# Optimization experiments

Hardware: AMD Instinct MI355X
Metric: run time of the kernel (lower is better)

## Reference

```python
import jax, jax.numpy as jnp
import numpy as np

TOP_K = 2
NUM_EXPERTS = 8
CAPACITY_FACTOR = 1.0


def setup_inputs() -> dict:
    key = jax.random.key(0)
    k1, k2, k3, k4 = jax.random.split(key, 4)
    sl, bs, hs, ffn = 2048, 2, 1024, 4096
    x = jax.random.normal(k1, (sl, bs, hs), dtype=jnp.float32)
    router_w = jax.random.normal(k2, (hs, NUM_EXPERTS), dtype=jnp.float32) * 0.02
    w1 = jax.random.normal(k3, (NUM_EXPERTS, hs, ffn), dtype=jnp.float32) * 0.02
    w2 = jax.random.normal(k4, (NUM_EXPERTS, ffn, hs), dtype=jnp.float32) * 0.02
    bias = jnp.zeros((1, 1, hs), dtype=jnp.float32)
    return {"x": x, "router_w": router_w, "w1": w1, "w2": w2, "bias": bias}


def _moe_forward(x, router_w, w1, w2):
    sl, bs, hs = x.shape
    xf = x.reshape(-1, hs)                                   # [T, H]
    T = xf.shape[0]
    TK = T * TOP_K
    capacity = int(CAPACITY_FACTOR * TOP_K * T / NUM_EXPERTS)  # static

    # Router: softmax over experts, then top-k (LearnedRouter)
    scores = jax.nn.softmax(xf @ router_w, axis=-1)          # [T, E]
    expert_weights, top_experts = jax.lax.top_k(scores, TOP_K)  # [T, K]
    ew = expert_weights.reshape(-1)                          # [T*K]
    te = top_experts.reshape(-1).astype(jnp.int32)           # [T*K]

    # indices_and_bins: stable sort by expert id + histogram + inclusive cumsum
    indices = jnp.argsort(te, stable=True)                   # sorted pos -> flat slot
    tokens_per_expert = jnp.zeros((NUM_EXPERTS,), jnp.int32).at[te].add(1)
    bins = jnp.cumsum(tokens_per_expert)                     # inclusive cumsum
    starts = bins - tokens_per_expert                        # exclusive offsets

    # binned_gather -> [E, capacity, H]; tokens beyond capacity are dropped
    c_range = jnp.arange(capacity)
    pos = starts[:, None] + c_range[None, :]                 # [E, C] positions in sorted order
    valid = c_range[None, :] < tokens_per_expert[:, None]    # [E, C]
    slot = indices[jnp.clip(pos, 0, TK - 1)]                 # flat (token*K + k) slot
    tok = slot // TOP_K                                      # source token row
    gathered = jnp.where(valid[..., None], xf[tok], 0.0)     # [E, C, H]

    # grouped expert MLP: gelu(x @ w1) @ w2  (megablocks mlp.MLP)
    h = jax.nn.gelu(jnp.einsum('ech,ehf->ecf', gathered, w1))
    y = jnp.einsum('ecf,efh->ech', h, w2)                    # [E, C, H]

    # binned_scatter: weighted accumulate back to token rows
    p = jnp.arange(TK)
    e_of_p = jnp.searchsorted(bins, p, side='right')         # expert of sorted pos
    c_of_p = p - starts[e_of_p]                              # slot within expert bin
    ok = c_of_p < capacity                                   # dropped tokens contribute 0
    vals = jnp.where(ok[:, None], y[e_of_p, jnp.clip(c_of_p, 0, capacity - 1)], 0.0)
    flat = indices                                           # flat slot at sorted pos p
    w = ew[flat]
    out = jnp.zeros((T, hs), x.dtype).at[flat // TOP_K].add(w[:, None] * vals)
    return out.reshape(sl, bs, hs)


def reference(x, router_w, w1, w2, bias):
    out = _moe_forward(x, router_w, w1, w2)
    return (out, bias)
```

## Files before the change

### kernel.cpp

```cpp
#include <hip/hip_runtime.h>
#include <hip/hip_bf16.h>


#define T_TOK 4096
#define HS 1024
#define FFN 4096
#define NE 8
#define CAP 1024
#define TKS 8192

#define WS_TE   67108864
#define WS_EW   67141632
#define WS_PERM 67174400
#define WS_WT   67239936
#define WS_XB   134348800

typedef float f4 __attribute__((ext_vector_type(4)));
typedef __bf16 bf16x8 __attribute__((ext_vector_type(8)));
typedef float f32x4 __attribute__((ext_vector_type(4)));

__device__ __forceinline__ void gld_lds16(const void* g, void* l) {
    __builtin_amdgcn_global_load_lds(
        (const __attribute__((address_space(1))) unsigned int*)g,
        (__attribute__((address_space(3))) unsigned int*)l, 16, 0, 0);
}

__global__ void init_out_kernel(float* __restrict__ out, const float* __restrict__ bias) {
    int i = blockIdx.x * 256 + threadIdx.x;
    const int TH = T_TOK * HS;
    if (i < TH) out[i] = 0.0f;
    else if (i < TH + HS) out[i] = bias[i - TH];
}

__global__ __launch_bounds__(256) void router_kernel(const float* __restrict__ x,
                                                     const float* __restrict__ rw,
                                                     int* __restrict__ te,
                                                     float* __restrict__ ew,
                                                     __bf16* __restrict__ xb) {
    __shared__ float rwt[NE * HS];
    int tid = threadIdx.x;
    for (int i = tid; i < NE * HS; i += 256) {
        int h = i >> 3, e = i & 7;
        rwt[e * HS + h] = rw[i];
    }
    __syncthreads();
    int wave = tid >> 6, lane = tid & 63;
    int t = blockIdx.x * 4 + wave;
    const float* xr = x + (size_t)t * HS;
    float s[NE];
    float xv[16];
#pragma unroll
    for (int e = 0; e < NE; ++e) s[e] = 0.0f;
#pragma unroll
    for (int j = 0; j < 16; ++j) {
        int h = lane + j * 64;
        xv[j] = xr[h];
#pragma unroll
        for (int e = 0; e < NE; ++e) s[e] += xv[j] * rwt[e * HS + h];
    }
#pragma unroll
    for (int j = 0; j < 16; ++j)
        xb[(size_t)t * HS + lane + j * 64] = (__bf16)xv[j];
#pragma unroll
    for (int e = 0; e < NE; ++e) {
#pragma unroll
        for (int off = 1; off < 64; off <<= 1) s[e] += __shfl_xor(s[e], off, 64);
    }
    float m = s[0];
#pragma unroll
    for (int e = 1; e < NE; ++e) m = fmaxf(m, s[e]);
    float psum = 0.0f;
#pragma unroll
    for (int e = 0; e < NE; ++e) psum += __expf(s[e] - m);
    int e0 = 0; float v0 = s[0];
#pragma unroll
    for (int e = 1; e < NE; ++e) { if (s[e] > v0) { v0 = s[e]; e0 = e; } }
    int e1 = -1; float v1 = -1e30f;
#pragma unroll
    for (int e = 0; e < NE; ++e) { if (e != e0 && s[e] > v1) { v1 = s[e]; e1 = e; } }
    if (lane == 0) {
        float inv = 1.0f / psum;
        te[2 * t]     = e0;
        te[2 * t + 1] = e1;
        ew[2 * t]     = __expf(v0 - m) * inv;
        ew[2 * t + 1] = __expf(v1 - m) * inv;
    }
}

__global__ __launch_bounds__(256) void sort_kernel(const int* __restrict__ te,
                                                   int* __restrict__ perm) {
    __shared__ int hist[256 * NE];
    int tid = threadIdx.x;
#pragma unroll
    for (int e = 0; e < NE; ++e) hist[tid * NE + e] = 0;
    for (int i = tid; i < TKS; i += 256) perm[i] = -1;
    __syncthreads();
    for (int j = 0; j < 32; ++j) {
        int p = tid * 32 + j;
        hist[tid * NE + te[p]]++;
    }
    __syncthreads();
    if (tid < NE) {
        int run = 0;
        for (int i = 0; i < 256; ++i) {
            int v = hist[i * NE + tid];
            hist[i * NE + tid] = run;
            run += v;
        }
    }
    __syncthreads();
    for (int j = 0; j < 32; ++j) {
        int p = tid * 32 + j;
        int e = te[p];
        int c = hist[tid * NE + e]++;
        if (c < CAP) perm[e * CAP + c] = p;
    }
}

__global__ __launch_bounds__(256) void conv_wt_kernel(const float* __restrict__ w,
                                                      __bf16* __restrict__ wt,
                                                      int K, int N) {
    __shared__ __bf16 t[64][72];
    const int e = blockIdx.z;
    const int kb = blockIdx.y * 64, nb = blockIdx.x * 64;
    const int tid = threadIdx.x;
    const float* src = w + ((size_t)e * K + kb) * N + nb;
    {
        const int kk = tid >> 4, nc = (tid & 15) * 4;
#pragma unroll
        for (int i = 0; i < 4; ++i) {
            int k = kk + 16 * i;
            f4 v = *(const f4*)(src + (size_t)k * N + nc);
            t[nc + 0][k] = (__bf16)v[0];
            t[nc + 1][k] = (__bf16)v[1];
            t[nc + 2][k] = (__bf16)v[2];
            t[nc + 3][k] = (__bf16)v[3];
        }
    }
    __syncthreads();
    __bf16* dst = wt + ((size_t)e * N + nb) * K + kb;
    const int nn = tid >> 3, ch = (tid & 7) * 8;
#pragma unroll
    for (int i = 0; i < 2; ++i) {
        int n = nn + 32 * i;
        bf16x8 v = *(const bf16x8*)(&t[n][ch]);
        *(bf16x8*)(dst + (size_t)n * K + ch) = v;
    }
}


#define PBAR() do {                                                         \
    asm volatile("" ::: "memory");                                          \
    __builtin_amdgcn_s_barrier();                                           \
    asm volatile("" ::: "memory");                                          \
} while (0)

#define WAITV(N_) asm volatile("s_waitcnt vmcnt(" #N_ ")" ::: "memory")

#define STAGE_A(cb_, h_, koff_) do {                                        \
    gld_lds16(aptr[(h_)*2 + 0] + (koff_), &As[cb_][(h_)*128 + w*16 + 0][0]);\
    gld_lds16(aptr[(h_)*2 + 1] + (koff_), &As[cb_][(h_)*128 + w*16 + 8][0]);\
} while (0)

#define STAGE_B(cb_, h_, koff_) do {                                        \
    gld_lds16(bptr[(h_)*2 + 0] + (koff_), &Bs[cb_][(h_)*128 + w*16 + 0][0]);\
    gld_lds16(bptr[(h_)*2 + 1] + (koff_), &Bs[cb_][(h_)*128 + w*16 + 8][0]);\
} while (0)

#define RD_A4(MB_) do {                                                     \
    _Pragma("unroll")                                                       \
    for (int mi = 0; mi < 4; ++mi)                                          \
        _Pragma("unroll")                                                   \
        for (int kk = 0; kk < 2; ++kk)                                      \
            a[mi][kk] = *(const bf16x8*)&As[c][wr*128 + ((MB_)+mi)*16 + l15]\
                            [((kk*4 + (lane>>4)) ^ (lane&7)) * 8];          \
} while (0)

#define RD_B2(NB_) do {                                                     \
    _Pragma("unroll")                                                       \
    for (int ni = 0; ni < 2; ++ni)                                          \
        _Pragma("unroll")                                                   \
        for (int kk = 0; kk < 2; ++kk)                                      \
            b[(NB_)+ni][kk] = *(const bf16x8*)&Bs[c][wc*64 + ((NB_)+ni)*16 + l15]\
                            [((kk*4 + (lane>>4)) ^ (lane&7)) * 8];          \
} while (0)

#define MFMA16(MB_, NB_) do {                                               \
    __builtin_amdgcn_s_setprio(1);                                          \
    _Pragma("unroll")                                                       \
    for (int mi = 0; mi < 4; ++mi)                                          \
        _Pragma("unroll")                                                   \
        for (int ni = 0; ni < 2; ++ni)                                      \
            _Pragma("unroll")                                               \
            for (int kk = 0; kk < 2; ++kk)                                  \
                acc[(MB_)+mi][(NB_)+ni] = __builtin_amdgcn_mfma_f32_16x16x32_bf16(\
                    a[mi][kk], b[(NB_)+ni][kk], acc[(MB_)+mi][(NB_)+ni], 0, 0, 0);\
    __builtin_amdgcn_s_setprio(0);                                          \
} while (0)

#define KLOOP(NT_)                                                          \
    STAGE_A(0, 0, 0); STAGE_A(0, 1, 0);                                     \
    STAGE_B(0, 0, 0); STAGE_B(0, 1, 0);                                     \
    STAGE_A(1, 0, 64); STAGE_A(1, 1, 64);                                   \
    for (int t = 0; t < (NT_); ++t) {                                       \
        const int c = t & 1;                                                \
        if (t == (NT_) - 1) WAITV(0); else WAITV(4);                        \
        PBAR();                                                             \
                                                               \
        RD_A4(0); RD_B2(0);                                                 \
        if (t + 1 < (NT_)) STAGE_B(c ^ 1, 0, (t + 1) * 64);                 \
        PBAR();                                                             \
        MFMA16(0, 0);                                                       \
        PBAR();                                                             \
                                                               \
        RD_B2(2);                                                           \
        if (t + 1 < (NT_)) STAGE_B(c ^ 1, 1, (t + 1) * 64);                 \
        PBAR();                                                             \
        MFMA16(0, 2);                                                       \
        PBAR();                                                             \
                                                               \
        RD_A4(4);                                                           \
        PBAR();                                                             \
        MFMA16(4, 2);                                                       \
        PBAR();                                                             \
                                                               \
        if (t + 2 < (NT_)) { STAGE_A(c, 0, (t + 2) * 64);                   \
                             STAGE_A(c, 1, (t + 2) * 64); }                 \
        PBAR();                                                             \
        __builtin_amdgcn_sched_barrier(0);                                  \
        MFMA16(4, 0);                                                       \
        PBAR();                                                             \
    }

__global__ __launch_bounds__(512, 2) void gemm1_kernel(const __bf16* __restrict__ xb,
                                                       const __bf16* __restrict__ w1t,
                                                       const int* __restrict__ perm,
                                                       __bf16* __restrict__ hbuf) {
    __shared__ __bf16 As[2][256][64];
    __shared__ __bf16 Bs[2][256][64];
    const int e = blockIdx.z, mblk = blockIdx.y, nblk = blockIdx.x;
    const int tid = threadIdx.x, lane = tid & 63, w = tid >> 6;
    const int wr = w >> 2, wc = w & 3;
    const int l15 = lane & 15;
    const int srl = lane >> 3;
    const int gsrc = (lane & 7) ^ srl;

    const __bf16* aptr[4];
    const __bf16* bptr[4];
#pragma unroll
    for (int h = 0; h < 2; ++h) {
#pragma unroll
        for (int o = 0; o < 2; ++o) {
            int r = h * 128 + w * 16 + o * 8 + srl;
            int p = perm[e * CAP + mblk * 256 + r];
            int tok = (p < 0) ? 0 : (p >> 1);
            aptr[h * 2 + o] = xb + (size_t)tok * HS + gsrc * 8;
            int brow = nblk * 256 + r;
            bptr[h * 2 + o] = w1t + ((size_t)e * FFN + brow) * HS + gsrc * 8;
        }
    }

    f32x4 acc[8][4];
#pragma unroll
    for (int mi = 0; mi < 8; ++mi)
#pragma unroll
        for (int ni = 0; ni < 4; ++ni) acc[mi][ni] = (f32x4)0.0f;
    bf16x8 a[4][2], b[4][2];

    KLOOP(HS / 64)

    const int mbase = mblk * 256 + wr * 128;
    const int nbase = nblk * 256 + wc * 64;
#pragma unroll
    for (int mi = 0; mi < 8; ++mi) {
#pragma unroll
        for (int ni = 0; ni < 4; ++ni) {
#pragma unroll
            for (int reg = 0; reg < 4; ++reg) {
                int mrow = mbase + mi * 16 + (lane >> 4) * 4 + reg;
                int ncol = nbase + ni * 16 + l15;
                float z = acc[mi][ni][reg];
                float z2 = z * z;
                float y = z * (1.5957691216057308f + 0.07135481627f * z2);
                float ex = __expf(-y);
                float gv = z * __builtin_amdgcn_rcpf(1.0f + ex);
                hbuf[(size_t)(e * CAP + mrow) * FFN + ncol] = (__bf16)gv;
            }
        }
    }
}

__global__ __launch_bounds__(512, 2) void gemm2_kernel(const __bf16* __restrict__ hbuf,
                                                       const __bf16* __restrict__ w2t,
                                                       const int* __restrict__ perm,
                                                       const float* __restrict__ ew,
                                                       float* __restrict__ out) {
    __shared__ __bf16 As[2][256][64];
    __shared__ __bf16 Bs[2][256][64];
    const int e = blockIdx.z & 7, half = blockIdx.z >> 3;
    const int mblk = blockIdx.y, nblk = blockIdx.x;
    const int tid = threadIdx.x, lane = tid & 63, w = tid >> 6;
    const int wr = w >> 2, wc = w & 3;
    const int l15 = lane & 15;
    const int srl = lane >> 3;
    const int gsrc = (lane & 7) ^ srl;
    const size_t kbase = (size_t)half * 2048;

    const __bf16* aptr[4];
    const __bf16* bptr[4];
#pragma unroll
    for (int h = 0; h < 2; ++h) {
#pragma unroll
        for (int o = 0; o < 2; ++o) {
            int r = h * 128 + w * 16 + o * 8 + srl;
            aptr[h * 2 + o] = hbuf + ((size_t)(e * CAP + mblk * 256 + r)) * FFN
                              + kbase + gsrc * 8;
            int brow = nblk * 256 + r;
            bptr[h * 2 + o] = w2t + ((size_t)e * HS + brow) * FFN
                              + kbase + gsrc * 8;
        }
    }

    f32x4 acc[8][4];
#pragma unroll
    for (int mi = 0; mi < 8; ++mi)
#pragma unroll
        for (int ni = 0; ni < 4; ++ni) acc[mi][ni] = (f32x4)0.0f;
    bf16x8 a[4][2], b[4][2];

    KLOOP(2048 / 64)

    __syncthreads();
    int* sperm = (int*)&As[0][0][0];
    float* swt = (float*)(sperm + 256);
    if (tid < 256) {
        int p = perm[e * CAP + mblk * 256 + tid];
        sperm[tid] = p;
        swt[tid] = (p >= 0) ? ew[p] : 0.0f;
    }
    __syncthreads();

    const int nbase = nblk * 256 + wc * 64;
#pragma unroll
    for (int mi = 0; mi < 8; ++mi) {
#pragma unroll
        for (int reg = 0; reg < 4; ++reg) {
            int mloc = wr * 128 + mi * 16 + (lane >> 4) * 4 + reg;
            int p = sperm[mloc];
            if (p >= 0) {
                int tok = p >> 1;
                float wgt = swt[mloc];
#pragma unroll
                for (int ni = 0; ni < 4; ++ni) {
                    int n = nbase + ni * 16 + l15;
                    atomicAdd(&out[(size_t)tok * HS + n], wgt * acc[mi][ni][reg]);
                }
            }
        }
    }
}

extern "C" void kernel_launch(void* const* d_in, const int* in_sizes, int n_in,
                              void* d_out, int out_size, void* d_ws, size_t ws_size,
                              hipStream_t stream) {
    const float* x    = (const float*)d_in[0];
    const float* rw   = (const float*)d_in[1];
    const float* w1   = (const float*)d_in[2];
    const float* w2   = (const float*)d_in[3];
    const float* bias = (const float*)d_in[4];
    float* out = (float*)d_out;
    char* ws = (char*)d_ws;

    __bf16* hbuf = (__bf16*)ws;
    int*    te   = (int*)(ws + WS_TE);
    float*  ew   = (float*)(ws + WS_EW);
    int*    perm = (int*)(ws + WS_PERM);
    __bf16* wt   = (__bf16*)(ws + WS_WT);
    __bf16* xb   = (__bf16*)(ws + WS_XB);

    hipLaunchKernelGGL(init_out_kernel, dim3((T_TOK * HS + HS + 255) / 256), dim3(256),
                       0, stream, out, bias);
    hipLaunchKernelGGL(router_kernel, dim3(T_TOK / 4), dim3(256), 0, stream,
                       x, rw, te, ew, xb);
    hipLaunchKernelGGL(sort_kernel, dim3(1), dim3(256), 0, stream, te, perm);
    hipLaunchKernelGGL(conv_wt_kernel, dim3(FFN / 64, HS / 64, NE), dim3(256),
                       0, stream, w1, wt, HS, FFN);
    hipLaunchKernelGGL(gemm1_kernel, dim3(FFN / 256, CAP / 256, NE), dim3(512),
                       0, stream, xb, wt, perm, hbuf);
    hipLaunchKernelGGL(conv_wt_kernel, dim3(HS / 64, FFN / 64, NE), dim3(256),
                       0, stream, w2, wt, FFN, HS);
    hipLaunchKernelGGL(gemm2_kernel, dim3(HS / 256, CAP / 256, NE * 2), dim3(512),
                       0, stream, hbuf, wt, perm, ew, out);
}
```

Baseline: 289.1 us.

## Restructure GEMM K-loop prefetch and remap blocks to XCDs by expert

The K-loop now stages a full A+B tile two iterations ahead in one place, replacing the split staging of B one tile ahead and A two ahead. It removes two barriers per iteration and adjusts the vmcnt wait to match the larger number of outstanding loads. Both GEMM kernels also remap the hardware block index so that consecutive blocks dispatched round-robin across the 8 XCDs map to the same expert and weight slice, aiming for better L2 reuse. Dropping the trailing barrier is risky: the next iteration's stage into the buffer just read relies on the barrier at the top of the following iteration.

Result: no change. 290.3 us (+0.4%).

```diff
diff --git a/kernel.cpp b/kernel.cpp
--- a/kernel.cpp
+++ b/kernel.cpp
@@ -165,6 +165,11 @@
 #define STAGE_B(cb_, h_, koff_) do {                                        \
     gld_lds16(bptr[(h_)*2 + 0] + (koff_), &Bs[cb_][(h_)*128 + w*16 + 0][0]);\
     gld_lds16(bptr[(h_)*2 + 1] + (koff_), &Bs[cb_][(h_)*128 + w*16 + 8][0]);\
+} while (0)
+
+#define STAGE_TILE(cb_, koff_) do {                                         \
+    STAGE_A(cb_, 0, koff_); STAGE_A(cb_, 1, koff_);                         \
+    STAGE_B(cb_, 0, koff_); STAGE_B(cb_, 1, koff_);                         \
 } while (0)
 
 #define RD_A4(MB_) do {                                                     \
@@ -199,22 +204,19 @@
 } while (0)
 
 #define KLOOP(NT_)                                                          \
-    STAGE_A(0, 0, 0); STAGE_A(0, 1, 0);                                     \
-    STAGE_B(0, 0, 0); STAGE_B(0, 1, 0);                                     \
-    STAGE_A(1, 0, 64); STAGE_A(1, 1, 64);                                   \
+    STAGE_TILE(0, 0);                                                       \
+    STAGE_TILE(1, 64);                                                      \
     for (int t = 0; t < (NT_); ++t) {                                       \
         const int c = t & 1;                                                \
-        if (t == (NT_) - 1) WAITV(0); else WAITV(4);                        \
+        if (t == (NT_) - 1) WAITV(0); else WAITV(8);                        \
         PBAR();                                                             \
                                                                \
         RD_A4(0); RD_B2(0);                                                 \
-        if (t + 1 < (NT_)) STAGE_B(c ^ 1, 0, (t + 1) * 64);                 \
         PBAR();                                                             \
         MFMA16(0, 0);                                                       \
         PBAR();                                                             \
                                                                \
         RD_B2(2);                                                           \
-        if (t + 1 < (NT_)) STAGE_B(c ^ 1, 1, (t + 1) * 64);                 \
         PBAR();                                                             \
         MFMA16(0, 2);                                                       \
         PBAR();                                                             \
@@ -223,13 +225,10 @@
         PBAR();                                                             \
         MFMA16(4, 2);                                                       \
         PBAR();                                                             \
-                                                               \
-        if (t + 2 < (NT_)) { STAGE_A(c, 0, (t + 2) * 64);                   \
-                             STAGE_A(c, 1, (t + 2) * 64); }                 \
-        PBAR();                                                             \
+               \
+        if (t + 2 < (NT_)) STAGE_TILE(c, (t + 2) * 64);                     \
         __builtin_amdgcn_sched_barrier(0);                                  \
         MFMA16(4, 0);                                                       \
-        PBAR();                                                             \
     }
 
 __global__ __launch_bounds__(512, 2) void gemm1_kernel(const __bf16* __restrict__ xb,
@@ -238,7 +237,11 @@
                                                        __bf16* __restrict__ hbuf) {
     __shared__ __bf16 As[2][256][64];
     __shared__ __bf16 Bs[2][256][64];
-    const int e = blockIdx.z, mblk = blockIdx.y, nblk = blockIdx.x;
+    const int hw = blockIdx.x + 16 * blockIdx.y + 64 * blockIdx.z;
+    const int logical = (hw & 7) * 64 + (hw >> 3);
+    const int nblk = logical & 15;
+    const int mblk = (logical >> 4) & 3;
+    const int e    = logical >> 6;
     const int tid = threadIdx.x, lane = tid & 63, w = tid >> 6;
     const int wr = w >> 2, wc = w & 3;
     const int l15 = lane & 15;
@@ -297,8 +300,12 @@
                                                        float* __restrict__ out) {
     __shared__ __bf16 As[2][256][64];
     __shared__ __bf16 Bs[2][256][64];
-    const int e = blockIdx.z & 7, half = blockIdx.z >> 3;
-    const int mblk = blockIdx.y, nblk = blockIdx.x;
+    const int hw = blockIdx.x + 4 * blockIdx.y + 16 * blockIdx.z;
+    const int logical = (hw & 7) * 32 + (hw >> 3);
+    const int nblk = logical & 3;
+    const int mblk = (logical >> 2) & 3;
+    const int zz   = logical >> 4;
+    const int e    = zz >> 1, half = zz & 1;
     const int tid = threadIdx.x, lane = tid & 63, w = tid >> 6;
     const int wr = w >> 2, wc = w & 3;
     const int l15 = lane & 15;
```
